# Optimization experiments

Measured on AMD Instinct MI355X. Metric: run time of the kernel, lower is better.

The kernel has to match this reference:

```python
import jax, jax.numpy as jnp
import numpy as np

N_P, N_A, N_S, D = 50000, 25000, 1, 64
ALPHA = 0.2  # leaky_relu negative slope
E_P2P, E_P2A, E_A2P, E_A2A = 800000, 400000, 400000, 400000


def _gat(z_msg, wh_dst, aw, src, dst, n_dst):
    """Per-edge-type GAT: score = leaky_relu(attn_fc([z_src ; Wh_dst])),
    segment softmax over destination, weighted scatter-sum of z_src.
    Attention linear is split into src/dst halves and applied per-node (cheaper)."""
    d = z_msg.shape[1]
    e = (z_msg @ aw[:d])[src] + (wh_dst @ aw[d:])[dst]  # [E]
    e = jnp.where(e > 0, e, ALPHA * e)                   # leaky_relu
    m = jax.ops.segment_max(e, dst, num_segments=n_dst)
    ex = jnp.exp(e - m[dst])
    den = jax.ops.segment_sum(ex, dst, num_segments=n_dst)
    w = ex / den[dst]                                    # per-dst softmax (mailbox softmax)
    return jax.ops.segment_sum(w[:, None] * z_msg[src], dst, num_segments=n_dst)


def setup_inputs() -> dict:
    ks = jax.random.split(jax.random.key(0), 32)
    sc = 1.0 / np.sqrt(D)
    f32, i32 = jnp.float32, jnp.int32
    inp = {
        "feat_P": jax.random.normal(ks[0], (N_P, D), f32),
        "feat_A": jax.random.normal(ks[1], (N_A, D), f32),
        "feat_state": jax.random.normal(ks[2], (N_S, D), f32),
    }
    for i, n in enumerate(["P", "A", "p2p", "p2a", "a2p", "a2a", "p2s", "a2s", "in"]):
        inp["W_" + n] = jax.random.normal(ks[3 + i], (D, D), f32) * sc
        inp["b_" + n] = jnp.zeros((D,), f32)
    for i, n in enumerate(["p2p", "p2a", "a2p", "a2a", "p2s", "a2s"]):
        inp["a_" + n] = jax.random.normal(ks[12 + i], (2 * D,), f32) * sc
    inp["src_p2p"] = jax.random.randint(ks[18], (E_P2P,), 0, N_P, i32)
    inp["dst_p2p"] = jax.random.randint(ks[19], (E_P2P,), 0, N_P, i32)
    inp["src_p2a"] = jax.random.randint(ks[20], (E_P2A,), 0, N_P, i32)
    inp["dst_p2a"] = jax.random.randint(ks[21], (E_P2A,), 0, N_A, i32)
    inp["src_a2p"] = jax.random.randint(ks[22], (E_A2P,), 0, N_A, i32)
    inp["dst_a2p"] = jax.random.randint(ks[23], (E_A2P,), 0, N_P, i32)
    inp["src_a2a"] = jax.random.randint(ks[24], (E_A2A,), 0, N_A, i32)
    inp["dst_a2a"] = jax.random.randint(ks[25], (E_A2A,), 0, N_A, i32)
    inp["src_p2s"] = jnp.arange(N_P, dtype=i32)
    inp["dst_p2s"] = jnp.zeros((N_P,), i32)
    inp["src_a2s"] = jnp.arange(N_A, dtype=i32)
    inp["dst_a2s"] = jnp.zeros((N_A,), i32)
    return inp


def reference(feat_P, feat_A, feat_state,
              W_P, b_P, W_A, b_A, W_p2p, b_p2p, W_p2a, b_p2a, W_a2p, b_a2p,
              W_a2a, b_a2a, W_p2s, b_p2s, W_a2s, b_a2s, W_in, b_in,
              a_p2p, a_p2a, a_a2p, a_a2a, a_p2s, a_a2s,
              src_p2p, dst_p2p, src_p2a, dst_p2a, src_a2p, dst_a2p,
              src_a2a, dst_a2a, src_p2s, dst_p2s, src_a2s, dst_a2s):
    Wh_P = feat_P @ W_P + b_P          # self transform per node type
    Wh_A = feat_A @ W_A + b_A
    Wh_in = feat_state @ W_in + b_in   # 'in' self-loop message to state
    h_P = jax.nn.relu(
        Wh_P
        + _gat(feat_P @ W_p2p + b_p2p, Wh_P, a_p2p, src_p2p, dst_p2p, N_P)
        + _gat(feat_A @ W_a2p + b_a2p, Wh_P, a_a2p, src_a2p, dst_a2p, N_P))
    h_A = jax.nn.relu(
        Wh_A
        + _gat(feat_P @ W_p2a + b_p2a, Wh_A, a_p2a, src_p2a, dst_p2a, N_A)
        + _gat(feat_A @ W_a2a + b_a2a, Wh_A, a_a2a, src_a2a, dst_a2a, N_A))
    h_S = jax.nn.relu(
        Wh_in
        + _gat(feat_P @ W_p2s + b_p2s, Wh_in, a_p2s, src_p2s, dst_p2s, N_S)
        + _gat(feat_A @ W_a2s + b_a2s, Wh_in, a_a2s, src_a2s, dst_a2s, N_S))
    return (h_P, h_A, h_S)
```

## Files before the change

### kernel.cpp

```cpp
#include <hip/hip_runtime.h>
#include <math.h>

#define ALPHA 0.2f
#define NP 50000
#define NA 25000
#define NBINS 150000
#define ABASE 100000
#define NBUCK 586
#define CH 4096
#define CAP 8192
#define GP ((NP + 63) / 64)
#define GA ((NA + 63) / 64)
#define GATB ((NP + NA) / 4)
#define SNB_P 128
#define SNB_A 64
#define SNB (SNB_P + SNB_A)

typedef unsigned short u16;
typedef __attribute__((ext_vector_type(8))) short bf16x8;
typedef __attribute__((ext_vector_type(8))) unsigned short u16x8;
typedef __attribute__((ext_vector_type(4))) float f32x4;

__device__ __forceinline__ float bf2f(u16 u) { return __uint_as_float(((unsigned)u) << 16); }
__device__ __forceinline__ u16 f2bf(float f) {
    unsigned x = __float_as_uint(f);
    return (u16)((x + 0x7fffu + ((x >> 16) & 1u)) >> 16);
}

struct FrontArgs {
    const float *feat_P, *feat_A, *feat_S;
    const float *W_P, *b_P, *W_A, *b_A, *W_p2p, *b_p2p, *W_p2a, *b_p2a,
                *W_a2p, *b_a2p, *W_a2a, *b_a2a, *W_p2s, *b_p2s, *W_a2s, *b_a2s,
                *W_in, *b_in;
    const float *a_p2p, *a_p2a, *a_a2p, *a_a2a, *a_p2s, *a_a2s;
    float *WhP, *WhA;
    u16 *z_p2p, *z_p2a, *z_p2s, *z_a2p, *z_a2a, *z_a2s;
    float *ss_p2p, *sd_p2p, *ss_p2a, *sd_p2a, *ss_a2p, *sd_a2p, *ss_a2a, *sd_a2a,
          *ss_p2s, *ss_a2s;
    float *sdst2, *outS, *den2, *numP, *numA;
    int *done;
    const int *src_p2p, *dst_p2p, *src_a2p, *dst_a2p,
              *src_p2a, *dst_p2a, *src_a2a, *dst_a2a;
    int E_p2p, E_a2p, E_p2a, E_a2a, E_tot, nblk;
    int *cursor0, *ebuf;
};

__device__ __forceinline__ void xform_body(int bid,
    const float* __restrict__ X, int N,
    const float* __restrict__ W0, const float* __restrict__ b0, float* __restrict__ Wh,
    const float* __restrict__ dA, float* __restrict__ sdA,
    const float* __restrict__ dB, float* __restrict__ sdB,
    const float* __restrict__ W1, const float* __restrict__ b1, u16* __restrict__ z1,
    const float* __restrict__ v1, float* __restrict__ s1,
    const float* __restrict__ W2, const float* __restrict__ b2, u16* __restrict__ z2,
    const float* __restrict__ v2, float* __restrict__ s2,
    const float* __restrict__ W3, const float* __restrict__ b3, u16* __restrict__ z3,
    const float* __restrict__ v3, float* __restrict__ s3)
{
    int tid = threadIdx.x, wv = tid >> 6, lane = tid & 63;
    int g = lane >> 4, li = lane & 15;
    const float* Wm = wv == 0 ? W0 : wv == 1 ? W1 : wv == 2 ? W2 : W3;
    const float* bm = wv == 0 ? b0 : wv == 1 ? b1 : wv == 2 ? b2 : b3;
    const float* dv = wv == 0 ? dA : wv == 1 ? v1 : wv == 2 ? v2 : v3;
    float* sm       = wv == 0 ? sdA : wv == 1 ? s1 : wv == 2 ? s2 : s3;
    u16* zm         = wv == 1 ? z1 : wv == 2 ? z2 : wv == 3 ? z3 : nullptr;

    bf16x8 Bf[4][2];
#pragma unroll
    for (int cb = 0; cb < 4; ++cb)
#pragma unroll
        for (int kc = 0; kc < 2; ++kc) {
            bf16x8 t;
#pragma unroll
            for (int j = 0; j < 8; ++j)
                t[j] = (short)f2bf(Wm[(kc * 32 + g * 8 + j) * 64 + cb * 16 + li]);
            Bf[cb][kc] = t;
        }
    float bl[4], dvl[4], dbl[4];
#pragma unroll
    for (int cb = 0; cb < 4; ++cb) {
        bl[cb]  = bm[cb * 16 + li];
        dvl[cb] = dv[cb * 16 + li];
        dbl[cb] = (wv == 0) ? dB[cb * 16 + li] : 0.f;
    }

    int base0 = bid * 64;
#pragma unroll
    for (int rt = 0; rt < 4; ++rt) {
        int rbase = base0 + rt * 16;
        if (rbase >= N) break;
        int rowC = min(rbase + li, N - 1);
        bf16x8 Af[2];
#pragma unroll
        for (int kc = 0; kc < 2; ++kc) {
            const float* xp = X + (long long)rowC * 64 + kc * 32 + g * 8;
            float4 x0 = *(const float4*)xp;
            float4 x1 = *(const float4*)(xp + 4);
            bf16x8 t;
            t[0] = (short)f2bf(x0.x); t[1] = (short)f2bf(x0.y);
            t[2] = (short)f2bf(x0.z); t[3] = (short)f2bf(x0.w);
            t[4] = (short)f2bf(x1.x); t[5] = (short)f2bf(x1.y);
            t[6] = (short)f2bf(x1.z); t[7] = (short)f2bf(x1.w);
            Af[kc] = t;
        }
        f32x4 acc[4] = {{0,0,0,0},{0,0,0,0},{0,0,0,0},{0,0,0,0}};
#pragma unroll
        for (int kc = 0; kc < 2; ++kc)
#pragma unroll
            for (int cb = 0; cb < 4; ++cb)
                acc[cb] = __builtin_amdgcn_mfma_f32_16x16x32_bf16(Af[kc], Bf[cb][kc], acc[cb], 0, 0, 0);
        float pd[4] = {0,0,0,0}, pb[4] = {0,0,0,0};
#pragma unroll
        for (int cb = 0; cb < 4; ++cb)
#pragma unroll
            for (int r = 0; r < 4; ++r) {
                float val = acc[cb][r] + bl[cb];
                acc[cb][r] = val;
                pd[r] = fmaf(val, dvl[cb], pd[r]);
                pb[r] = fmaf(val, dbl[cb], pb[r]);
            }
#pragma unroll
        for (int o = 1; o < 16; o <<= 1)
#pragma unroll
            for (int r = 0; r < 4; ++r) {
                pd[r] += __shfl_xor(pd[r], o, 64);
                pb[r] += __shfl_xor(pb[r], o, 64);
            }
        int rg = rbase + g * 4;
        if (li == 0) {
#pragma unroll
            for (int r = 0; r < 4; ++r) {
                int row = rg + r;
                if (row < N) {
                    sm[row] = pd[r];
                    if (wv == 0) sdB[row] = pb[r];
                }
            }
        }
        if (wv == 0) {
#pragma unroll
            for (int r = 0; r < 4; ++r) {
                int row = rg + r;
                if (row < N)
#pragma unroll
                    for (int cb = 0; cb < 4; ++cb)
                        Wh[(long long)row * 64 + cb * 16 + li] = acc[cb][r];
            }
        } else {
#pragma unroll
            for (int r = 0; r < 4; ++r) {
                int row = rg + r;
                if (row < N)
#pragma unroll
                    for (int cb = 0; cb < 4; ++cb)
                        zm[(long long)row * 64 + cb * 16 + li] = f2bf(acc[cb][r]);
            }
        }
    }
}

__device__ __forceinline__ void edge_decode(int k,
    const int* __restrict__ s0, const int* __restrict__ d0, int E0,
    const int* __restrict__ s1, const int* __restrict__ d1, int E1,
    const int* __restrict__ s2, const int* __restrict__ d2, int E2,
    const int* __restrict__ s3, const int* __restrict__ d3,
    int& src, int& bin) {
    if (k < E0) { src = s0[k]; bin = 2 * d0[k]; return; }
    k -= E0; if (k < E1) { src = s1[k]; bin = 2 * d1[k] + 1; return; }
    k -= E1; if (k < E2) { src = s2[k]; bin = ABASE + 2 * d2[k]; return; }
    k -= E2; src = s3[k]; bin = ABASE + 2 * d3[k] + 1;
}

__global__ __launch_bounds__(256) void fused_front(FrontArgs A) {
    __shared__ int h[NBUCK];
    __shared__ int base[NBUCK];
    int bid = blockIdx.x;
    int tid = threadIdx.x;
    if (bid < A.nblk) {
        for (int i = tid; i < NBUCK; i += 256) h[i] = 0;
        __syncthreads();
        int b0 = bid * CH;
        int b1 = min(b0 + CH, A.E_tot);
        int cbin[16], csrc[16];
#pragma unroll
        for (int it = 0; it < 16; ++it) {
            int i = b0 + it * 256 + tid;
            int bin = -1, src = 0;
            if (i < b1)
                edge_decode(i, A.src_p2p, A.dst_p2p, A.E_p2p,
                            A.src_a2p, A.dst_a2p, A.E_a2p,
                            A.src_p2a, A.dst_p2a, A.E_p2a,
                            A.src_a2a, A.dst_a2a, src, bin);
            cbin[it] = bin; csrc[it] = src;
            if (bin >= 0) atomicAdd(&h[bin >> 8], 1);
        }
        __syncthreads();
        for (int i = tid; i < NBUCK; i += 256) {
            int c = h[i];
            base[i] = c ? (i * CAP + atomicAdd(&A.cursor0[i], c)) : 0;
            h[i] = 0;
        }
        __syncthreads();
#pragma unroll
        for (int it = 0; it < 16; ++it) {
            int bin = cbin[it];
            if (bin >= 0) {
                int bk = bin >> 8;
                int pos = base[bk] + atomicAdd(&h[bk], 1);
                if (pos < (bk + 1) * CAP)
                    A.ebuf[pos] = csrc[it] | ((bin & 255) << 16);
            }
        }
        return;
    }
    bid -= A.nblk;
    if (bid < GP) {
        xform_body(bid, A.feat_P, NP,
                   A.W_P, A.b_P, A.WhP, A.a_p2p + 64, A.sd_p2p, A.a_a2p + 64, A.sd_a2p,
                   A.W_p2p, A.b_p2p, A.z_p2p, A.a_p2p, A.ss_p2p,
                   A.W_p2a, A.b_p2a, A.z_p2a, A.a_p2a, A.ss_p2a,
                   A.W_p2s, A.b_p2s, A.z_p2s, A.a_p2s, A.ss_p2s);
        return;
    }
    bid -= GP;
    if (bid < GA) {
        xform_body(bid, A.feat_A, NA,
                   A.W_A, A.b_A, A.WhA, A.a_p2a + 64, A.sd_p2a, A.a_a2a + 64, A.sd_a2a,
                   A.W_a2p, A.b_a2p, A.z_a2p, A.a_a2p, A.ss_a2p,
                   A.W_a2a, A.b_a2a, A.z_a2a, A.a_a2a, A.ss_a2a,
                   A.W_a2s, A.b_a2s, A.z_a2s, A.a_a2s, A.ss_a2s);
        return;
    }
    if (tid < 64) {
        int c = tid;
        float acc = A.b_in[c];
        for (int k = 0; k < 64; ++k) acc = fmaf(A.feat_S[k], A.W_in[k * 64 + c], acc);
        A.outS[c] = acc;
        float v0 = acc * A.a_p2s[64 + c];
        float v1 = acc * A.a_a2s[64 + c];
#pragma unroll
        for (int off = 32; off > 0; off >>= 1) {
            v0 += __shfl_down(v0, off, 64);
            v1 += __shfl_down(v1, off, 64);
        }
        if (c == 0) { A.sdst2[0] = v0; A.sdst2[1] = v1; }
    } else if (tid < 128) A.numP[tid - 64] = 0.f;
    else if (tid < 192)   A.numA[tid - 128] = 0.f;
    else if (tid == 192)  A.den2[0] = 0.f;
    else if (tid == 193)  A.den2[1] = 0.f;
    else if (tid == 194)  *A.done = 0;
}

__device__ void scan_counts(const int* __restrict__ counts, int* sstart) {
    __shared__ int wtot_sb[4];
    int tid = threadIdx.x, lane = tid & 63, wv = tid >> 6;
    int carry = 0;
    for (int c = 0; c < 3; ++c) {
        int i = c * 256 + tid;
        int v = (i < NBUCK) ? min(counts[i], CAP) : 0;
        int x = v;
#pragma unroll
        for (int o = 1; o < 64; o <<= 1) {
            int y = __shfl_up(x, o, 64);
            if (lane >= o) x += y;
        }
        if (lane == 63) wtot_sb[wv] = x;
        __syncthreads();
        int woff = carry;
        for (int j = 0; j < wv; ++j) woff += wtot_sb[j];
        int ctot = wtot_sb[0] + wtot_sb[1] + wtot_sb[2] + wtot_sb[3];
        if (i < NBUCK) sstart[i] = x + woff - v;
        __syncthreads();
        carry += ctot;
    }
    if (tid == 0) sstart[NBUCK] = carry;
    __syncthreads();
}

__global__ __launch_bounds__(256) void fine_sort(
    const int* __restrict__ ebuf, const int* __restrict__ cursor0,
    int* __restrict__ ssrc, int* __restrict__ offs) {
    __shared__ int sstart[NBUCK + 1];
    __shared__ int lsrc[CAP];
    __shared__ int lcnt[256];
    __shared__ int loff[256];
    __shared__ int lcur[256];
    __shared__ int wtot[4];
    int b = blockIdx.x;
    int tid = threadIdx.x, lane = tid & 63, wv = tid >> 6;
    scan_counts(cursor0, sstart);
    int pstart = sstart[b];
    int rstart = b * CAP;
    int cnt = min(cursor0[b], CAP);
    lcnt[tid] = 0;
    __syncthreads();
    for (int e = tid; e < cnt; e += 256)
        atomicAdd(&lcnt[((unsigned)ebuf[rstart + e]) >> 16], 1);
    __syncthreads();
    int v = lcnt[tid];
    int x = v;
#pragma unroll
    for (int o = 1; o < 64; o <<= 1) {
        int y = __shfl_up(x, o, 64);
        if (lane >= o) x += y;
    }
    if (lane == 63) wtot[wv] = x;
    __syncthreads();
    int woff = 0;
    for (int j = 0; j < wv; ++j) woff += wtot[j];
    int excl = x + woff - v;
    loff[tid] = excl;
    lcur[tid] = excl;
    __syncthreads();
    for (int e = tid; e < cnt; e += 256) {
        int val = ebuf[rstart + e];
        int pos = atomicAdd(&lcur[((unsigned)val) >> 16], 1);
        lsrc[pos] = val & 0xFFFF;
    }
    __syncthreads();
    for (int i = tid; i < cnt; i += 256) ssrc[pstart + i] = lsrc[i];
    int gb = b * 256 + tid;
    if (gb < NBINS) offs[gb] = pstart + loff[tid];
    if (b == 0 && tid == 0) offs[NBINS] = sstart[NBUCK];
}

__device__ __forceinline__ void seg_gat_g8(const int* __restrict__ ssrc, int s0, int s1,
                                           const float* __restrict__ ss, float sd,
                                           const u16* __restrict__ z, int lane,
                                           float* __restrict__ acc) {
    int cnt = s1 - s0;
    if (cnt <= 0) return;
    int egrp = lane >> 3, cg8 = (lane & 7) * 8;
    if (cnt <= 64) {
        int s = 0; float w = 0.f;
        if (lane < cnt) {
            s = ssrc[s0 + lane];
            float e = ss[s] + sd;
            e = e > 0.f ? e : ALPHA * e;
            w = __expf(e);
        }
        float den = w;
#pragma unroll
        for (int o = 32; o > 0; o >>= 1) den += __shfl_xor(den, o, 64);
        w *= 1.f / den;
        int nit = (cnt + 7) >> 3;
        for (int it = 0; it < nit; ++it) {
            int ei = it * 8 + egrp;
            float wt = __shfl(w, ei, 64);
            int   st = __shfl(s, ei, 64);
            u16x8 q = *(const u16x8*)(z + (long long)st * 64 + cg8);
#pragma unroll
            for (int j = 0; j < 8; ++j)
                acc[j] = fmaf(wt, bf2f(q[j]), acc[j]);
        }
    } else {
        float den = 0.f;
        for (int i = s0 + lane; i < s1; i += 64) {
            float e = ss[ssrc[i]] + sd; e = e > 0.f ? e : ALPHA * e; den += __expf(e);
        }
#pragma unroll
        for (int o = 32; o > 0; o >>= 1) den += __shfl_xor(den, o, 64);
        float inv = 1.f / den;
        for (int c = s0; c < s1; c += 64) {
            int i = c + lane; int s = 0; float w = 0.f;
            if (i < s1) {
                s = ssrc[i];
                float e = ss[s] + sd; e = e > 0.f ? e : ALPHA * e;
                w = __expf(e) * inv;
            }
            int cc = min(64, s1 - c);
            int nit = (cc + 7) >> 3;
            for (int it = 0; it < nit; ++it) {
                int ei = it * 8 + egrp;
                float wt = __shfl(w, ei, 64);
                int   st = __shfl(s, ei, 64);
                u16x8 q = *(const u16x8*)(z + (long long)st * 64 + cg8);
#pragma unroll
                for (int j = 0; j < 8; ++j)
                    acc[j] = fmaf(wt, bf2f(q[j]), acc[j]);
            }
        }
    }
}

__global__ __launch_bounds__(256) void fused_back(
    const int* __restrict__ ssrc, const int* __restrict__ offs,
    const float* __restrict__ WhP, float* __restrict__ outP,
    const float* __restrict__ WhA, float* __restrict__ outA,
    const float* __restrict__ ss_p2p, const float* __restrict__ sd_p2p, const u16* __restrict__ z_p2p,
    const float* __restrict__ ss_a2p, const float* __restrict__ sd_a2p, const u16* __restrict__ z_a2p,
    const float* __restrict__ ss_p2a, const float* __restrict__ sd_p2a, const u16* __restrict__ z_p2a,
    const float* __restrict__ ss_a2a, const float* __restrict__ sd_a2a, const u16* __restrict__ z_a2a,
    const int* __restrict__ srcP, const float* __restrict__ ssP, const u16* __restrict__ zP, int EP,
    const int* __restrict__ srcA, const float* __restrict__ ssA, const u16* __restrict__ zA, int EA,
    const float* __restrict__ sdst2, float* __restrict__ numP, float* __restrict__ numA,
    float* __restrict__ den2, int* __restrict__ done, float* __restrict__ outS) {
    int tid = threadIdx.x, lane = tid & 63, wv = tid >> 6;
    if ((int)blockIdx.x >= SNB) {
        int g = ((int)blockIdx.x - SNB) * 4 + wv;
        bool isP = g < NP;
        int d = isP ? g : g - NP;
        int bin0 = isP ? 2 * d : ABASE + 2 * d;
        int2 e01 = *(const int2*)&offs[bin0];
        int e2 = offs[bin0 + 2];
        const float* ss0 = isP ? ss_p2p : ss_p2a;
        const float* ss1 = isP ? ss_a2p : ss_a2a;
        const u16* z0 = isP ? z_p2p : z_p2a;
        const u16* z1 = isP ? z_a2p : z_a2a;
        float sd0v = (isP ? sd_p2p : sd_p2a)[d];
        float sd1v = (isP ? sd_a2p : sd_a2a)[d];
        float acc[8] = {0.f, 0.f, 0.f, 0.f, 0.f, 0.f, 0.f, 0.f};
        seg_gat_g8(ssrc, e01.x, e01.y, ss0, sd0v, z0, lane, acc);
        seg_gat_g8(ssrc, e01.y, e2, ss1, sd1v, z1, lane, acc);
#pragma unroll
        for (int o = 8; o <= 32; o <<= 1)
#pragma unroll
            for (int j = 0; j < 8; ++j)
                acc[j] += __shfl_xor(acc[j], o, 64);
        if (lane < 8) {
            const float* Wh = isP ? WhP : WhA;
            float* outp = isP ? outP : outA;
            const float* sp = &Wh[(long long)d * 64 + lane * 8];
            float4 s0v = *(const float4*)sp;
            float4 s1v = *(const float4*)(sp + 4);
            float4 r0, r1;
            r0.x = fmaxf(s0v.x + acc[0], 0.f); r0.y = fmaxf(s0v.y + acc[1], 0.f);
            r0.z = fmaxf(s0v.z + acc[2], 0.f); r0.w = fmaxf(s0v.w + acc[3], 0.f);
            r1.x = fmaxf(s1v.x + acc[4], 0.f); r1.y = fmaxf(s1v.y + acc[5], 0.f);
            r1.z = fmaxf(s1v.z + acc[6], 0.f); r1.w = fmaxf(s1v.w + acc[7], 0.f);
            float* op = &outp[(long long)d * 64 + lane * 8];
            *(float4*)op = r0;
            *(float4*)(op + 4) = r1;
        }
        return;
    }
    __shared__ float red[4][64];
    __shared__ float dred[4];
    __shared__ int tick;
    int sb = blockIdx.x;
    bool isP = sb < SNB_P;
    const int* src = isP ? srcP : srcA;
    const float* ss = isP ? ssP : ssA;
    const u16* z = isP ? zP : zA;
    int E = isP ? EP : EA;
    float sdst = sdst2[isP ? 0 : 1];
    float* num = isP ? numP : numA;
    int bidl = isP ? sb : sb - SNB_P;
    int nb = isP ? SNB_P : SNB_A;
    int egrp = lane >> 3, cg8 = (lane & 7) * 8;
    int gw = bidl * 4 + wv;
    int waves = nb * 4;
    float acc[8] = {0,0,0,0,0,0,0,0};
    float dpart = 0.f;
    for (int base = gw * 8; base < E; base += waves * 8) {
        int i = base + egrp;
        float w = 0.f; int ri = 0;
        if (i < E) {
            ri = src[i];
            float e = ss[ri] + sdst;
            e = e > 0.f ? e : ALPHA * e;
            w = __expf(e);
        }
        dpart += w;
        u16x8 q = *(const u16x8*)(z + (long long)ri * 64 + cg8);
#pragma unroll
        for (int j = 0; j < 8; ++j)
            acc[j] = fmaf(w, bf2f(q[j]), acc[j]);
    }
#pragma unroll
    for (int o = 8; o <= 32; o <<= 1)
#pragma unroll
        for (int j = 0; j < 8; ++j)
            acc[j] += __shfl_xor(acc[j], o, 64);
#pragma unroll
    for (int o = 32; o > 0; o >>= 1) dpart += __shfl_xor(dpart, o, 64);
    if (lane < 8)
#pragma unroll
        for (int j = 0; j < 8; ++j) red[wv][lane * 8 + j] = acc[j];
    if (lane == 0) dred[wv] = dpart;
    __syncthreads();
    if (tid < 64) {
        float t = red[0][tid] + red[1][tid] + red[2][tid] + red[3][tid];
        atomicAdd(&num[tid], t);
    }
    if (tid == 64) {
        float dtot = (dred[0] + dred[1] + dred[2] + dred[3]) * 0.125f;
        atomicAdd(&den2[isP ? 0 : 1], dtot);
    }
    __threadfence();
    __syncthreads();
    if (tid == 0) tick = atomicAdd(done, 1);
    __syncthreads();
    if (tick == SNB - 1 && tid < 64) {
        float dP = __hip_atomic_load(&den2[0], __ATOMIC_ACQUIRE, __HIP_MEMORY_SCOPE_AGENT);
        float dA = __hip_atomic_load(&den2[1], __ATOMIC_ACQUIRE, __HIP_MEMORY_SCOPE_AGENT);
        float nP = __hip_atomic_load(&numP[tid], __ATOMIC_ACQUIRE, __HIP_MEMORY_SCOPE_AGENT);
        float nA = __hip_atomic_load(&numA[tid], __ATOMIC_ACQUIRE, __HIP_MEMORY_SCOPE_AGENT);
        float whin = outS[tid];
        outS[tid] = fmaxf(whin + nP / dP + nA / dA, 0.f);
    }
}

extern "C" void kernel_launch(void* const* d_in, const int* in_sizes, int n_in,
                              void* d_out, int out_size, void* d_ws, size_t ws_size,
                              hipStream_t stream) {
    const float* feat_P = (const float*)d_in[0];
    const float* feat_A = (const float*)d_in[1];
    const float* feat_S = (const float*)d_in[2];
    const float* W_P   = (const float*)d_in[3];  const float* b_P   = (const float*)d_in[4];
    const float* W_A   = (const float*)d_in[5];  const float* b_A   = (const float*)d_in[6];
    const float* W_p2p = (const float*)d_in[7];  const float* b_p2p = (const float*)d_in[8];
    const float* W_p2a = (const float*)d_in[9];  const float* b_p2a = (const float*)d_in[10];
    const float* W_a2p = (const float*)d_in[11]; const float* b_a2p = (const float*)d_in[12];
    const float* W_a2a = (const float*)d_in[13]; const float* b_a2a = (const float*)d_in[14];
    const float* W_p2s = (const float*)d_in[15]; const float* b_p2s = (const float*)d_in[16];
    const float* W_a2s = (const float*)d_in[17]; const float* b_a2s = (const float*)d_in[18];
    const float* W_in  = (const float*)d_in[19]; const float* b_in  = (const float*)d_in[20];
    const float* a_p2p = (const float*)d_in[21];
    const float* a_p2a = (const float*)d_in[22];
    const float* a_a2p = (const float*)d_in[23];
    const float* a_a2a = (const float*)d_in[24];
    const float* a_p2s = (const float*)d_in[25];
    const float* a_a2s = (const float*)d_in[26];
    const int* src_p2p = (const int*)d_in[27]; const int* dst_p2p = (const int*)d_in[28];
    const int* src_p2a = (const int*)d_in[29]; const int* dst_p2a = (const int*)d_in[30];
    const int* src_a2p = (const int*)d_in[31]; const int* dst_a2p = (const int*)d_in[32];
    const int* src_a2a = (const int*)d_in[33]; const int* dst_a2a = (const int*)d_in[34];
    const int* src_p2s = (const int*)d_in[35];
    const int* src_a2s = (const int*)d_in[37];
    int E_p2p = in_sizes[27], E_p2a = in_sizes[29], E_a2p = in_sizes[31], E_a2a = in_sizes[33];
    int E_p2s = in_sizes[35], E_a2s = in_sizes[37];
    int E_tot = E_p2p + E_a2p + E_p2a + E_a2a;

    float* out = (float*)d_out;
    float* outP = out;
    float* outA = out + (long long)NP * 64;
    float* outS = out + (long long)(NP + NA) * 64;

    float* ws = (float*)d_ws;
    float* WhP = ws; ws += (long long)NP * 64;
    float* WhA = ws; ws += (long long)NA * 64;
    u16* z_p2p = (u16*)ws; ws += (long long)NP * 32;
    u16* z_p2a = (u16*)ws; ws += (long long)NP * 32;
    u16* z_p2s = (u16*)ws; ws += (long long)NP * 32;
    u16* z_a2p = (u16*)ws; ws += (long long)NA * 32;
    u16* z_a2a = (u16*)ws; ws += (long long)NA * 32;
    u16* z_a2s = (u16*)ws; ws += (long long)NA * 32;
    float* ss_p2p = ws; ws += NP;  float* sd_p2p = ws; ws += NP;
    float* ss_p2a = ws; ws += NP;  float* sd_p2a = ws; ws += NA;
    float* ss_a2p = ws; ws += NA;  float* sd_a2p = ws; ws += NP;
    float* ss_a2a = ws; ws += NA;  float* sd_a2a = ws; ws += NA;
    float* ss_p2s = ws; ws += NP;
    float* ss_a2s = ws; ws += NA;
    float* sdst2  = ws; ws += 2;
    float* den2   = ws; ws += 2;
    float* numP   = ws; ws += 64;
    float* numA   = ws; ws += 64;
    int*   done   = (int*)ws; ws += 1;
    int* cursor0 = (int*)ws; ws += NBUCK;
    int* iw = (int*)ws;
    int* ebuf = iw; iw += NBUCK * CAP;
    int* ssrc = iw; iw += E_tot;
    int* offs = iw; iw += NBINS + 1;

    const int T = 256;
    int nblk = (E_tot + CH - 1) / CH;

    hipMemsetAsync(cursor0, 0, (size_t)NBUCK * 4, stream);

    FrontArgs FA;
    FA.feat_P = feat_P; FA.feat_A = feat_A; FA.feat_S = feat_S;
    FA.W_P = W_P; FA.b_P = b_P; FA.W_A = W_A; FA.b_A = b_A;
    FA.W_p2p = W_p2p; FA.b_p2p = b_p2p; FA.W_p2a = W_p2a; FA.b_p2a = b_p2a;
    FA.W_a2p = W_a2p; FA.b_a2p = b_a2p; FA.W_a2a = W_a2a; FA.b_a2a = b_a2a;
    FA.W_p2s = W_p2s; FA.b_p2s = b_p2s; FA.W_a2s = W_a2s; FA.b_a2s = b_a2s;
    FA.W_in = W_in; FA.b_in = b_in;
    FA.a_p2p = a_p2p; FA.a_p2a = a_p2a; FA.a_a2p = a_a2p; FA.a_a2a = a_a2a;
    FA.a_p2s = a_p2s; FA.a_a2s = a_a2s;
    FA.WhP = WhP; FA.WhA = WhA;
    FA.z_p2p = z_p2p; FA.z_p2a = z_p2a; FA.z_p2s = z_p2s;
    FA.z_a2p = z_a2p; FA.z_a2a = z_a2a; FA.z_a2s = z_a2s;
    FA.ss_p2p = ss_p2p; FA.sd_p2p = sd_p2p; FA.ss_p2a = ss_p2a; FA.sd_p2a = sd_p2a;
    FA.ss_a2p = ss_a2p; FA.sd_a2p = sd_a2p; FA.ss_a2a = ss_a2a; FA.sd_a2a = sd_a2a;
    FA.ss_p2s = ss_p2s; FA.ss_a2s = ss_a2s;
    FA.sdst2 = sdst2; FA.outS = outS; FA.den2 = den2; FA.numP = numP; FA.numA = numA;
    FA.done = done;
    FA.src_p2p = src_p2p; FA.dst_p2p = dst_p2p; FA.src_a2p = src_a2p; FA.dst_a2p = dst_a2p;
    FA.src_p2a = src_p2a; FA.dst_p2a = dst_p2a; FA.src_a2a = src_a2a; FA.dst_a2a = dst_a2a;
    FA.E_p2p = E_p2p; FA.E_a2p = E_a2p; FA.E_p2a = E_p2a; FA.E_a2a = E_a2a;
    FA.E_tot = E_tot; FA.nblk = nblk;
    FA.cursor0 = cursor0; FA.ebuf = ebuf;
    fused_front<<<nblk + GP + GA + 1, T, 0, stream>>>(FA);

    fine_sort<<<NBUCK, T, 0, stream>>>(ebuf, cursor0, ssrc, offs);

    fused_back<<<SNB + GATB, T, 0, stream>>>(ssrc, offs,
        WhP, outP, WhA, outA,
        ss_p2p, sd_p2p, z_p2p, ss_a2p, sd_a2p, z_a2p,
        ss_p2a, sd_p2a, z_p2a, ss_a2a, sd_a2a, z_a2a,
        src_p2s, ss_p2s, z_p2s, E_p2s,
        src_a2s, ss_a2s, z_a2s, E_a2s,
        sdst2, numP, numA, den2, done, outS);
}
```

Baseline: 148.4 us.

## Move state-node reduction into sort kernel and split per-node GAT into own kernel

The state-node (p2s/a2s) reduction blocks now run inside the fine-sort launch, so those blocks overlap with the bucket sort instead of sharing a launch with the per-node GAT. The per-destination GAT becomes a separate lean kernel with fewer parameters and branch-specialised pointer selection. Kernel count stays at three, but the sort kernel's large shared-memory footprint now applies to the reduction blocks too, which may lower their occupancy.

```diff
diff --git a/kernel.cpp b/kernel.cpp
--- a/kernel.cpp
+++ b/kernel.cpp
@@ -11,7 +11,6 @@
 #define CAP 8192
 #define GP ((NP + 63) / 64)
 #define GA ((NA + 63) / 64)
-#define GATB ((NP + NA) / 4)
 #define SNB_P 128
 #define SNB_A 64
 #define SNB (SNB_P + SNB_A)
@@ -277,167 +276,62 @@
     __syncthreads();
 }
 
-__global__ __launch_bounds__(256) void fine_sort(
+__global__ __launch_bounds__(256) void fused_mid(
     const int* __restrict__ ebuf, const int* __restrict__ cursor0,
-    int* __restrict__ ssrc, int* __restrict__ offs) {
-    __shared__ int sstart[NBUCK + 1];
-    __shared__ int lsrc[CAP];
-    __shared__ int lcnt[256];
-    __shared__ int loff[256];
-    __shared__ int lcur[256];
-    __shared__ int wtot[4];
-    int b = blockIdx.x;
-    int tid = threadIdx.x, lane = tid & 63, wv = tid >> 6;
-    scan_counts(cursor0, sstart);
-    int pstart = sstart[b];
-    int rstart = b * CAP;
-    int cnt = min(cursor0[b], CAP);
-    lcnt[tid] = 0;
-    __syncthreads();
-    for (int e = tid; e < cnt; e += 256)
-        atomicAdd(&lcnt[((unsigned)ebuf[rstart + e]) >> 16], 1);
-    __syncthreads();
-    int v = lcnt[tid];
-    int x = v;
-#pragma unroll
-    for (int o = 1; o < 64; o <<= 1) {
-        int y = __shfl_up(x, o, 64);
-        if (lane >= o) x += y;
-    }
-    if (lane == 63) wtot[wv] = x;
-    __syncthreads();
-    int woff = 0;
-    for (int j = 0; j < wv; ++j) woff += wtot[j];
-    int excl = x + woff - v;
-    loff[tid] = excl;
-    lcur[tid] = excl;
-    __syncthreads();
-    for (int e = tid; e < cnt; e += 256) {
-        int val = ebuf[rstart + e];
-        int pos = atomicAdd(&lcur[((unsigned)val) >> 16], 1);
-        lsrc[pos] = val & 0xFFFF;
-    }
-    __syncthreads();
-    for (int i = tid; i < cnt; i += 256) ssrc[pstart + i] = lsrc[i];
-    int gb = b * 256 + tid;
-    if (gb < NBINS) offs[gb] = pstart + loff[tid];
-    if (b == 0 && tid == 0) offs[NBINS] = sstart[NBUCK];
-}
-
-__device__ __forceinline__ void seg_gat_g8(const int* __restrict__ ssrc, int s0, int s1,
-                                           const float* __restrict__ ss, float sd,
-                                           const u16* __restrict__ z, int lane,
-                                           float* __restrict__ acc) {
-    int cnt = s1 - s0;
-    if (cnt <= 0) return;
-    int egrp = lane >> 3, cg8 = (lane & 7) * 8;
-    if (cnt <= 64) {
-        int s = 0; float w = 0.f;
-        if (lane < cnt) {
-            s = ssrc[s0 + lane];
-            float e = ss[s] + sd;
-            e = e > 0.f ? e : ALPHA * e;
-            w = __expf(e);
-        }
-        float den = w;
-#pragma unroll
-        for (int o = 32; o > 0; o >>= 1) den += __shfl_xor(den, o, 64);
-        w *= 1.f / den;
-        int nit = (cnt + 7) >> 3;
-        for (int it = 0; it < nit; ++it) {
-            int ei = it * 8 + egrp;
-            float wt = __shfl(w, ei, 64);
-            int   st = __shfl(s, ei, 64);
-            u16x8 q = *(const u16x8*)(z + (long long)st * 64 + cg8);
-#pragma unroll
-            for (int j = 0; j < 8; ++j)
-                acc[j] = fmaf(wt, bf2f(q[j]), acc[j]);
-        }
-    } else {
-        float den = 0.f;
-        for (int i = s0 + lane; i < s1; i += 64) {
-            float e = ss[ssrc[i]] + sd; e = e > 0.f ? e : ALPHA * e; den += __expf(e);
-        }
-#pragma unroll
-        for (int o = 32; o > 0; o >>= 1) den += __shfl_xor(den, o, 64);
-        float inv = 1.f / den;
-        for (int c = s0; c < s1; c += 64) {
-            int i = c + lane; int s = 0; float w = 0.f;
-            if (i < s1) {
-                s = ssrc[i];
-                float e = ss[s] + sd; e = e > 0.f ? e : ALPHA * e;
-                w = __expf(e) * inv;
-            }
-            int cc = min(64, s1 - c);
-            int nit = (cc + 7) >> 3;
-            for (int it = 0; it < nit; ++it) {
-                int ei = it * 8 + egrp;
-                float wt = __shfl(w, ei, 64);
-                int   st = __shfl(s, ei, 64);
-                u16x8 q = *(const u16x8*)(z + (long long)st * 64 + cg8);
-#pragma unroll
-                for (int j = 0; j < 8; ++j)
-                    acc[j] = fmaf(wt, bf2f(q[j]), acc[j]);
-            }
-        }
-    }
-}
-
-__global__ __launch_bounds__(256) void fused_back(
-    const int* __restrict__ ssrc, const int* __restrict__ offs,
-    const float* __restrict__ WhP, float* __restrict__ outP,
-    const float* __restrict__ WhA, float* __restrict__ outA,
-    const float* __restrict__ ss_p2p, const float* __restrict__ sd_p2p, const u16* __restrict__ z_p2p,
-    const float* __restrict__ ss_a2p, const float* __restrict__ sd_a2p, const u16* __restrict__ z_a2p,
-    const float* __restrict__ ss_p2a, const float* __restrict__ sd_p2a, const u16* __restrict__ z_p2a,
-    const float* __restrict__ ss_a2a, const float* __restrict__ sd_a2a, const u16* __restrict__ z_a2a,
+    int* __restrict__ ssrc, int* __restrict__ offs,
     const int* __restrict__ srcP, const float* __restrict__ ssP, const u16* __restrict__ zP, int EP,
     const int* __restrict__ srcA, const float* __restrict__ ssA, const u16* __restrict__ zA, int EA,
     const float* __restrict__ sdst2, float* __restrict__ numP, float* __restrict__ numA,
     float* __restrict__ den2, int* __restrict__ done, float* __restrict__ outS) {
     int tid = threadIdx.x, lane = tid & 63, wv = tid >> 6;
-    if ((int)blockIdx.x >= SNB) {
-        int g = ((int)blockIdx.x - SNB) * 4 + wv;
-        bool isP = g < NP;
-        int d = isP ? g : g - NP;
-        int bin0 = isP ? 2 * d : ABASE + 2 * d;
-        int2 e01 = *(const int2*)&offs[bin0];
-        int e2 = offs[bin0 + 2];
-        const float* ss0 = isP ? ss_p2p : ss_p2a;
-        const float* ss1 = isP ? ss_a2p : ss_a2a;
-        const u16* z0 = isP ? z_p2p : z_p2a;
-        const u16* z1 = isP ? z_a2p : z_a2a;
-        float sd0v = (isP ? sd_p2p : sd_p2a)[d];
-        float sd1v = (isP ? sd_a2p : sd_a2a)[d];
-        float acc[8] = {0.f, 0.f, 0.f, 0.f, 0.f, 0.f, 0.f, 0.f};
-        seg_gat_g8(ssrc, e01.x, e01.y, ss0, sd0v, z0, lane, acc);
-        seg_gat_g8(ssrc, e01.y, e2, ss1, sd1v, z1, lane, acc);
-#pragma unroll
-        for (int o = 8; o <= 32; o <<= 1)
-#pragma unroll
-            for (int j = 0; j < 8; ++j)
-                acc[j] += __shfl_xor(acc[j], o, 64);
-        if (lane < 8) {
-            const float* Wh = isP ? WhP : WhA;
-            float* outp = isP ? outP : outA;
-            const float* sp = &Wh[(long long)d * 64 + lane * 8];
-            float4 s0v = *(const float4*)sp;
-            float4 s1v = *(const float4*)(sp + 4);
-            float4 r0, r1;
-            r0.x = fmaxf(s0v.x + acc[0], 0.f); r0.y = fmaxf(s0v.y + acc[1], 0.f);
-            r0.z = fmaxf(s0v.z + acc[2], 0.f); r0.w = fmaxf(s0v.w + acc[3], 0.f);
-            r1.x = fmaxf(s1v.x + acc[4], 0.f); r1.y = fmaxf(s1v.y + acc[5], 0.f);
-            r1.z = fmaxf(s1v.z + acc[6], 0.f); r1.w = fmaxf(s1v.w + acc[7], 0.f);
-            float* op = &outp[(long long)d * 64 + lane * 8];
-            *(float4*)op = r0;
-            *(float4*)(op + 4) = r1;
-        }
+    if ((int)blockIdx.x < NBUCK) {
+        __shared__ int sstart[NBUCK + 1];
+        __shared__ int lsrc[CAP];
+        __shared__ int lcnt[256];
+        __shared__ int loff[256];
+        __shared__ int lcur[256];
+        __shared__ int wtot[4];
+        int b = blockIdx.x;
+        scan_counts(cursor0, sstart);
+        int pstart = sstart[b];
+        int rstart = b * CAP;
+        int cnt = min(cursor0[b], CAP);
+        lcnt[tid] = 0;
+        __syncthreads();
+        for (int e = tid; e < cnt; e += 256)
+            atomicAdd(&lcnt[((unsigned)ebuf[rstart + e]) >> 16], 1);
+        __syncthreads();
+        int v = lcnt[tid];
+        int x = v;
+#pragma unroll
+        for (int o = 1; o < 64; o <<= 1) {
+            int y = __shfl_up(x, o, 64);
+            if (lane >= o) x += y;
+        }
+        if (lane == 63) wtot[wv] = x;
+        __syncthreads();
+        int woff = 0;
+        for (int j = 0; j < wv; ++j) woff += wtot[j];
+        int excl = x + woff - v;
+        loff[tid] = excl;
+        lcur[tid] = excl;
+        __syncthreads();
+        for (int e = tid; e < cnt; e += 256) {
+            int val = ebuf[rstart + e];
+            int pos = atomicAdd(&lcur[((unsigned)val) >> 16], 1);
+            lsrc[pos] = val & 0xFFFF;
+        }
+        __syncthreads();
+        for (int i = tid; i < cnt; i += 256) ssrc[pstart + i] = lsrc[i];
+        int gb = b * 256 + tid;
+        if (gb < NBINS) offs[gb] = pstart + loff[tid];
+        if (b == 0 && tid == 0) offs[NBINS] = sstart[NBUCK];
         return;
     }
     __shared__ float red[4][64];
     __shared__ float dred[4];
     __shared__ int tick;
-    int sb = blockIdx.x;
+    int sb = blockIdx.x - NBUCK;
     bool isP = sb < SNB_P;
     const int* src = isP ? srcP : srcA;
     const float* ss = isP ? ssP : ssA;
@@ -498,6 +392,110 @@
         float nA = __hip_atomic_load(&numA[tid], __ATOMIC_ACQUIRE, __HIP_MEMORY_SCOPE_AGENT);
         float whin = outS[tid];
         outS[tid] = fmaxf(whin + nP / dP + nA / dA, 0.f);
+    }
+}
+
+__device__ __forceinline__ void seg_gat_g8(const int* __restrict__ ssrc, int s0, int s1,
+                                           const float* __restrict__ ss, float sd,
+                                           const u16* __restrict__ z, int lane,
+                                           float* __restrict__ acc) {
+    int cnt = s1 - s0;
+    if (cnt <= 0) return;
+    int egrp = lane >> 3, cg8 = (lane & 7) * 8;
+    if (cnt <= 64) {
+        int s = 0; float w = 0.f;
+        if (lane < cnt) {
+            s = ssrc[s0 + lane];
+            float e = ss[s] + sd;
+            e = e > 0.f ? e : ALPHA * e;
+            w = __expf(e);
+        }
+        float den = w;
+#pragma unroll
+        for (int o = 32; o > 0; o >>= 1) den += __shfl_xor(den, o, 64);
+        w *= 1.f / den;
+        int nit = (cnt + 7) >> 3;
+        for (int it = 0; it < nit; ++it) {
+            int ei = it * 8 + egrp;
+            float wt = __shfl(w, ei, 64);
+            int   st = __shfl(s, ei, 64);
+            u16x8 q = *(const u16x8*)(z + (long long)st * 64 + cg8);
+#pragma unroll
+            for (int j = 0; j < 8; ++j)
+                acc[j] = fmaf(wt, bf2f(q[j]), acc[j]);
+        }
+    } else {
+        float den = 0.f;
+        for (int i = s0 + lane; i < s1; i += 64) {
+            float e = ss[ssrc[i]] + sd; e = e > 0.f ? e : ALPHA * e; den += __expf(e);
+        }
+#pragma unroll
+        for (int o = 32; o > 0; o >>= 1) den += __shfl_xor(den, o, 64);
+        float inv = 1.f / den;
+        for (int c = s0; c < s1; c += 64) {
+            int i = c + lane; int s = 0; float w = 0.f;
+            if (i < s1) {
+                s = ssrc[i];
+                float e = ss[s] + sd; e = e > 0.f ? e : ALPHA * e;
+                w = __expf(e) * inv;
+            }
+            int cc = min(64, s1 - c);
+            int nit = (cc + 7) >> 3;
+            for (int it = 0; it < nit; ++it) {
+                int ei = it * 8 + egrp;
+                float wt = __shfl(w, ei, 64);
+                int   st = __shfl(s, ei, 64);
+                u16x8 q = *(const u16x8*)(z + (long long)st * 64 + cg8);
+#pragma unroll
+                for (int j = 0; j < 8; ++j)
+                    acc[j] = fmaf(wt, bf2f(q[j]), acc[j]);
+            }
+        }
+    }
+}
+
+__global__ __launch_bounds__(256) void gat_all(
+    const int* __restrict__ ssrc, const int* __restrict__ offs,
+    const float* __restrict__ WhP, float* __restrict__ outP,
+    const float* __restrict__ WhA, float* __restrict__ outA,
+    const float* __restrict__ ss_p2p, const float* __restrict__ sd_p2p, const u16* __restrict__ z_p2p,
+    const float* __restrict__ ss_a2p, const float* __restrict__ sd_a2p, const u16* __restrict__ z_a2p,
+    const float* __restrict__ ss_p2a, const float* __restrict__ sd_p2a, const u16* __restrict__ z_p2a,
+    const float* __restrict__ ss_a2a, const float* __restrict__ sd_a2a, const u16* __restrict__ z_a2a) {
+    int lane = threadIdx.x & 63;
+    int g = (blockIdx.x * blockDim.x + threadIdx.x) >> 6;
+    if (g >= NP + NA) return;
+    bool isP = g < NP;
+    int d = isP ? g : g - NP;
+    int bin0 = isP ? 2 * d : ABASE + 2 * d;
+    int e0 = offs[bin0], e1 = offs[bin0 + 1], e2 = offs[bin0 + 2];
+    float acc[8] = {0.f, 0.f, 0.f, 0.f, 0.f, 0.f, 0.f, 0.f};
+    if (isP) {
+        seg_gat_g8(ssrc, e0, e1, ss_p2p, sd_p2p[d], z_p2p, lane, acc);
+        seg_gat_g8(ssrc, e1, e2, ss_a2p, sd_a2p[d], z_a2p, lane, acc);
+    } else {
+        seg_gat_g8(ssrc, e0, e1, ss_p2a, sd_p2a[d], z_p2a, lane, acc);
+        seg_gat_g8(ssrc, e1, e2, ss_a2a, sd_a2a[d], z_a2a, lane, acc);
+    }
+#pragma unroll
+    for (int o = 8; o <= 32; o <<= 1)
+#pragma unroll
+        for (int j = 0; j < 8; ++j)
+            acc[j] += __shfl_xor(acc[j], o, 64);
+    if (lane < 8) {
+        const float* Wh = isP ? WhP : WhA;
+        float* outp = isP ? outP : outA;
+        const float* sp = &Wh[(long long)d * 64 + lane * 8];
+        float4 s0v = *(const float4*)sp;
+        float4 s1v = *(const float4*)(sp + 4);
+        float4 r0, r1;
+        r0.x = fmaxf(s0v.x + acc[0], 0.f); r0.y = fmaxf(s0v.y + acc[1], 0.f);
+        r0.z = fmaxf(s0v.z + acc[2], 0.f); r0.w = fmaxf(s0v.w + acc[3], 0.f);
+        r1.x = fmaxf(s1v.x + acc[4], 0.f); r1.y = fmaxf(s1v.y + acc[5], 0.f);
+        r1.z = fmaxf(s1v.z + acc[6], 0.f); r1.w = fmaxf(s1v.w + acc[7], 0.f);
+        float* op = &outp[(long long)d * 64 + lane * 8];
+        *(float4*)op = r0;
+        *(float4*)(op + 4) = r1;
     }
 }
 
@@ -592,13 +590,13 @@
     FA.cursor0 = cursor0; FA.ebuf = ebuf;
     fused_front<<<nblk + GP + GA + 1, T, 0, stream>>>(FA);
 
-    fine_sort<<<NBUCK, T, 0, stream>>>(ebuf, cursor0, ssrc, offs);
-
-    fused_back<<<SNB + GATB, T, 0, stream>>>(ssrc, offs,
-        WhP, outP, WhA, outA,
-        ss_p2p, sd_p2p, z_p2p, ss_a2p, sd_a2p, z_a2p,
-        ss_p2a, sd_p2a, z_p2a, ss_a2a, sd_a2a, z_a2a,
+    fused_mid<<<NBUCK + SNB, T, 0, stream>>>(ebuf, cursor0, ssrc, offs,
         src_p2s, ss_p2s, z_p2s, E_p2s,
         src_a2s, ss_a2s, z_a2s, E_a2s,
         sdst2, numP, numA, den2, done, outS);
-}
+
+    gat_all<<<((NP + NA) * 64 + T - 1) / T, T, 0, stream>>>(ssrc, offs,
+        WhP, outP, WhA, outA,
+        ss_p2p, sd_p2p, z_p2p, ss_a2p, sd_a2p, z_a2p,
+        ss_p2a, sd_p2a, z_p2a, ss_a2a, sd_a2a, z_a2a);
+}
```

Result: no change. 147.0 us (-0.9%).
